# Kernel tuning notes

Hardware: AMD Instinct MI355X
Metric: run time of the kernel (lower is better)

Reference implementation:

```python
import jax, jax.numpy as jnp
import numpy as np
from jax import lax

# Dimensions (must match input_specs)
B, T, C = 2, 2048, 1024
H = 4 * C          # FFN hidden
E_RWKV, E_TRANS = 6, 2
E = E_RWKV + E_TRANS
LN_EPS = 1e-5


def layernorm(x, g, b):
    m = x.mean(-1, keepdims=True)
    v = ((x - m) ** 2).mean(-1, keepdims=True)
    return (x - m) * lax.rsqrt(v + LN_EPS) * g + b


def setup_inputs() -> dict:
    key = jax.random.key(0)
    ks = jax.random.split(key, 24)
    s = 0.02
    inp = {
        "x": jax.random.normal(ks[0], (B, T, C), jnp.float32),
        "v_first": jax.random.normal(ks[1], (B, T, C), jnp.float32),
        "winners": jax.random.randint(ks[2], (B, T, 2), 0, E),
        "capital_shares": jax.random.uniform(ks[3], (E,), jnp.float32),
        # LayerNorms
        "ln1_g": jnp.ones((C,), jnp.float32), "ln1_b": jnp.zeros((C,), jnp.float32),
        "ln2_g": jnp.ones((C,), jnp.float32), "ln2_b": jnp.zeros((C,), jnp.float32),
        # RWKV-style time-mix (simplified RWKV7_TimeMix)
        "Wr": s * jax.random.normal(ks[4], (C, C), jnp.float32),
        "Wk": s * jax.random.normal(ks[5], (C, C), jnp.float32),
        "Wv": s * jax.random.normal(ks[6], (C, C), jnp.float32),
        "Wo": s * jax.random.normal(ks[7], (C, C), jnp.float32),
        "w_decay": jax.random.normal(ks[8], (C,), jnp.float32),
        "g_v": jax.random.normal(ks[9], (C,), jnp.float32),
        # bridge: linear on concat(h, rwkv_state)
        "Wb": s * jax.random.normal(ks[10], (2 * C, C), jnp.float32),
        "bb": jnp.zeros((C,), jnp.float32),
        # 6 stacked SparseRWKVFFN experts: sigmoid(x Wr_r) * (relu(x Wk_r)^2 Wv_r)
        "Wk_r": s * jax.random.normal(ks[11], (E_RWKV, C, H), jnp.float32),
        "Wv_r": s * jax.random.normal(ks[12], (E_RWKV, H, C), jnp.float32),
        "Wr_r": s * jax.random.normal(ks[13], (E_RWKV, C, C), jnp.float32),
        # 2 stacked LinearTransformerExpert: gelu((h+prefix) W1) W2
        "W1_t": s * jax.random.normal(ks[14], (E_TRANS, C, H), jnp.float32),
        "W2_t": s * jax.random.normal(ks[15], (E_TRANS, H, C), jnp.float32),
    }
    return inp


def reference(x, v_first, winners, capital_shares,
              ln1_g, ln1_b, ln2_g, ln2_b,
              Wr, Wk, Wv, Wo, w_decay, g_v,
              Wb, bb, Wk_r, Wv_r, Wr_r, W1_t, W2_t):
    # ---- attention (simplified RWKV time-mix), returns per-token state ----
    h1 = layernorm(x, ln1_g, ln1_b)
    r = jax.nn.sigmoid(h1 @ Wr)                      # [B,T,C]
    k = h1 @ Wk
    v = h1 @ Wv
    v = v + (v_first - v) * jax.nn.sigmoid(g_v)      # value-residual mix
    w = jax.nn.sigmoid(w_decay)                      # per-channel decay [C]

    def step(s, kv):
        k_t, v_t = kv                                # [B,C] each
        s = w * s + k_t * v_t
        return s, s

    s0 = jnp.zeros((B, C), x.dtype)
    _, states = lax.scan(step, s0, (jnp.swapaxes(k, 0, 1), jnp.swapaxes(v, 0, 1)))
    states = jnp.swapaxes(states, 0, 1)              # rwkv_state [B,T,C]

    att_out = (r * states) @ Wo
    x = x + att_out
    h = layernorm(x, ln2_g, ln2_b)

    # ---- bridge prefix (flat over tokens, vectorized) ----
    bridge_prefix = jnp.concatenate([h, states], axis=-1) @ Wb + bb  # [B,T,C]

    # ---- experts computed densely, combined by top-2 gates ----
    # RWKV FFN experts
    a = jnp.square(jax.nn.relu(jnp.einsum('btc,ech->ebth', h, Wk_r)))     # [Er,B,T,H]
    rec = jax.nn.sigmoid(jnp.einsum('btc,ecd->ebtd', h, Wr_r))            # [Er,B,T,C]
    out_r = rec * jnp.einsum('ebth,ehc->ebtc', a, Wv_r)                   # [Er,B,T,C]
    # Linear-transformer experts consume the bridge prefix
    ht = h + bridge_prefix
    out_t = jnp.einsum('ebth,ehc->ebtc',
                       jax.nn.gelu(jnp.einsum('btc,ech->ebth', ht, W1_t)),
                       W2_t)                                              # [Et,B,T,C]
    all_out = jnp.concatenate([out_r, out_t], axis=0)                     # [E,B,T,C]

    # top-2 combine, each rank weighted 0.5 (use_market=False branch)
    gate = 0.5 * (jax.nn.one_hot(winners[..., 0], E, dtype=x.dtype)
                  + jax.nn.one_hot(winners[..., 1], E, dtype=x.dtype))    # [B,T,E]
    final_out = jnp.einsum('ebtc,bte->btc', all_out, gate)

    return x + final_out
```

## Files before the change

kernel.cpp:

```cpp
#include <hip/hip_runtime.h>

typedef unsigned short u16;
typedef __bf16 bf16x8 __attribute__((ext_vector_type(8)));
typedef float f32x4 __attribute__((ext_vector_type(4)));

__device__ __forceinline__ float bf2f(u16 u){ union{unsigned i;float f;}x; x.i=((unsigned)u)<<16; return x.f; }
__device__ __forceinline__ u16 f2bf(float f){ union{float f;unsigned i;}x; x.f=f; unsigned r = x.i + 0x7FFFu + ((x.i>>16)&1u); return (u16)(r>>16); }
__device__ __forceinline__ float sigm(float x){ return 1.f/(1.f+expf(-x)); }

struct __align__(8) U16x4 { u16 v[4]; };

__global__ void conv_t(const float* __restrict__ src, u16* __restrict__ dst, int K, int N){
  __shared__ u16 tile[64][72];
  const size_t mo = (size_t)blockIdx.z * (size_t)K * (size_t)N;
  src += mo; dst += mo;
  int k0 = blockIdx.x*64, n0 = blockIdx.y*64;
  int tid = threadIdx.x;
  #pragma unroll
  for (int it=0; it<4; ++it){
    int e = it*1024 + tid*4;
    int r = e>>6, c = e&63;
    float4 v = *(const float4*)(src + (size_t)(k0+r)*N + n0 + c);
    tile[r][c+0]=f2bf(v.x); tile[r][c+1]=f2bf(v.y); tile[r][c+2]=f2bf(v.z); tile[r][c+3]=f2bf(v.w);
  }
  __syncthreads();
  #pragma unroll
  for (int it=0; it<4; ++it){
    int e = it*1024 + tid*4;
    int n = e>>6, k = e&63;
    U16x4 o;
    #pragma unroll
    for (int j=0;j<4;++j) o.v[j] = tile[k+j][n];
    *(U16x4*)(dst + (size_t)(n0+n)*K + k0 + k) = o;
  }
}

__global__ void ln_k(const float* __restrict__ x, const float* __restrict__ g, const float* __restrict__ b,
                     u16* __restrict__ out, int ostride){
  int row = blockIdx.x, tid = threadIdx.x;
  float4 v = *(const float4*)(x + (size_t)row*1024 + tid*4);
  float s = v.x+v.y+v.z+v.w;
  float ss = v.x*v.x+v.y*v.y+v.z*v.z+v.w*v.w;
  #pragma unroll
  for (int o=32;o;o>>=1){ s += __shfl_down(s,o); ss += __shfl_down(ss,o); }
  __shared__ float sm[8];
  int lane = tid&63, wv = tid>>6;
  if (!lane){ sm[wv]=s; sm[4+wv]=ss; }
  __syncthreads();
  s = sm[0]+sm[1]+sm[2]+sm[3]; ss = sm[4]+sm[5]+sm[6]+sm[7];
  float mean = s*(1.f/1024.f);
  float var = ss*(1.f/1024.f) - mean*mean;
  float inv = rsqrtf(var + 1e-5f);
  U16x4 o;
  const float* vp = &v.x;
  #pragma unroll
  for (int j=0;j<4;++j){
    int c = tid*4+j;
    o.v[j] = f2bf((vp[j]-mean)*inv*g[c] + b[c]);
  }
  *(U16x4*)(out + (size_t)row*ostride + tid*4) = o;
}

__global__ void scan_p1(const u16* __restrict__ kbuf, const u16* __restrict__ vbuf,
                        const float* __restrict__ w_decay, float* __restrict__ carry){
  int c = blockIdx.x*256 + threadIdx.x;
  int chunk = blockIdx.y, b = blockIdx.z;
  float w = sigm(w_decay[c]);
  float s = 0.f;
  size_t idx = ((size_t)(b*2048 + chunk*64))*1024 + c;
  #pragma unroll 4
  for (int i=0;i<64;++i){ s = w*s + bf2f(kbuf[idx])*bf2f(vbuf[idx]); idx += 1024; }
  carry[((size_t)(b*32+chunk))*1024 + c] = s;
}
__global__ void scan_p2(const float* __restrict__ w_decay, const float* __restrict__ carry,
                        float* __restrict__ startv){
  int c = blockIdx.x*256 + threadIdx.x;
  int b = blockIdx.y;
  float w = sigm(w_decay[c]);
  float wL = w;
  #pragma unroll
  for (int i=0;i<6;++i) wL *= wL;
  float p = 0.f;
  for (int j=0;j<32;++j){
    size_t id = ((size_t)(b*32+j))*1024 + c;
    startv[id] = p;
    p = wL*p + carry[id];
  }
}
__global__ void scan_p3(const u16* __restrict__ kbuf, const u16* __restrict__ vbuf, const u16* __restrict__ rbuf,
                        const float* __restrict__ w_decay, const float* __restrict__ startv,
                        u16* __restrict__ rs, u16* __restrict__ hcat){
  int c = blockIdx.x*256 + threadIdx.x;
  int chunk = blockIdx.y, b = blockIdx.z;
  float w = sigm(w_decay[c]);
  float s = startv[((size_t)(b*32+chunk))*1024 + c];
  size_t t0 = (size_t)b*2048 + chunk*64;
  size_t idx = t0*1024 + c;
  size_t idx2 = t0*2048 + 1024 + c;
  for (int i=0;i<64;++i){
    s = w*s + bf2f(kbuf[idx])*bf2f(vbuf[idx]);
    rs[idx] = f2bf(bf2f(rbuf[idx]) * s);
    hcat[idx2] = f2bf(s);
    idx += 1024; idx2 += 2048;
  }
}

__global__ void route_count(const int* __restrict__ winners, int* __restrict__ offs, int* __restrict__ cursor){
  __shared__ int cnt[8];
  if (threadIdx.x < 8) cnt[threadIdx.x] = 0;
  __syncthreads();
  for (int p = threadIdx.x; p < 8192; p += 256) atomicAdd(&cnt[winners[p]&7], 1);
  __syncthreads();
  if (threadIdx.x == 0){
    int s = 0;
    #pragma unroll
    for (int e=0;e<8;++e){ offs[e]=s; s+=cnt[e]; }
    offs[8]=s;
  }
  if (threadIdx.x < 8) cursor[threadIdx.x] = 0;
}
__global__ void route_scatter(const int* __restrict__ winners, const int* __restrict__ offs,
                              int* __restrict__ cursor, int* __restrict__ idx_all){
  int p = blockIdx.x*256 + threadIdx.x;
  if (p < 8192){
    int e = winners[p]&7;
    int pos = offs[e] + atomicAdd(&cursor[e], 1);
    idx_all[pos] = p>>1;
  }
}

struct GArgs {
  const u16* A; const u16* B;
  long long lda, bstride;
  int K, N, Mdense, eBase;
  const int* offs; const int* idx_all;
  const float* x; const float* v_first; const float* g_v;
  u16* rbuf; u16* kbuf; u16* vbuf;
  float* out;
  const u16* hcat; const float* bb; u16* ht;
  u16* act; u16* rec;
};

#define GLL(gp, lp) __builtin_amdgcn_global_load_lds((const __attribute__((address_space(1))) void*)(gp), \
                                                     (__attribute__((address_space(3))) void*)(lp), 16, 0, 0)

template<int EPI, int GATHER>
__global__ __launch_bounds__(256,2) void gemm_k(GArgs g){
  int e = g.eBase + blockIdx.z;
  int rbase = 0, m = g.Mdense;
  if (g.offs){ rbase = g.offs[e]; m = g.offs[e+1] - rbase; }
  if ((int)blockIdx.y * 128 >= m) return;
  __shared__ char smem[65536];
  const int tid = threadIdx.x, lane = tid&63, wave = tid>>6;
  const int wr = wave>>1, wc = wave&1;

  int srow[4], scol[4];
  #pragma unroll
  for (int i=0;i<4;++i){
    srow[i] = i*32 + (tid>>3);
    scol[i] = ((((tid&7)*16) ^ ((srow[i]&7)<<4)) >> 1);
  }
  const u16* bBase[4];
  #pragma unroll
  for (int i=0;i<4;++i)
    bBase[i] = g.B + (long long)blockIdx.z*g.bstride
             + ((long long)blockIdx.x*128 + srow[i])*(long long)g.K + scol[i];

  int aOff[4][2], bOff[4][2];
  #pragma unroll
  for (int mm=0;mm<4;++mm){
    int rm = wr*64 + mm*16 + (lane&15);
    int rn = wc*64 + mm*16 + (lane&15);
    #pragma unroll
    for (int kk=0;kk<2;++kk){
      int X = kk*64 + (lane>>4)*16;
      aOff[mm][kk] = rm*128 + (X ^ ((rm&7)<<4));
      bOff[mm][kk] = 16384 + rn*128 + (X ^ ((rn&7)<<4));
    }
  }
  char* ldsA = smem + wave*1024;
  char* ldsB = smem + 16384 + wave*1024;
  const int nk = g.K >> 6;

  for (int mt = blockIdx.y; mt*128 < m; mt += gridDim.y){
    const u16* aSrc[4]; const u16* bSrc[4];
    #pragma unroll
    for (int i=0;i<4;++i){
      int grow = mt*128 + srow[i];
      int lr = grow < m ? grow : m-1;
      long long arow;
      if (GATHER) arow = g.idx_all[rbase + lr];
      else if (g.offs) arow = rbase + lr;
      else arow = grow;
      aSrc[i] = g.A + arow*g.lda + scol[i];
      bSrc[i] = bBase[i];
    }
    f32x4 acc[4][4];
    #pragma unroll
    for (int mm=0;mm<4;++mm)
      #pragma unroll
      for (int nn=0;nn<4;++nn)
        acc[mm][nn] = f32x4{0.f,0.f,0.f,0.f};

    #pragma unroll
    for (int i=0;i<4;++i){
      GLL(aSrc[i], ldsA + i*4096);
      GLL(bSrc[i], ldsB + i*4096);
      aSrc[i] += 64; bSrc[i] += 64;
    }
    int cur = 0;
    for (int ks=0; ks<nk; ++ks){
      if (ks+1 < nk){
        int nb = (cur^1)*32768;
        #pragma unroll
        for (int i=0;i<4;++i){
          GLL(aSrc[i], ldsA + nb + i*4096);
          GLL(bSrc[i], ldsB + nb + i*4096);
          aSrc[i] += 64; bSrc[i] += 64;
        }
        asm volatile("s_waitcnt vmcnt(8)" ::: "memory");
      } else {
        asm volatile("s_waitcnt vmcnt(0)" ::: "memory");
      }
      asm volatile("s_barrier" ::: "memory");
      const char* base = smem + cur*32768;
      #pragma unroll
      for (int kk=0;kk<2;++kk){
        bf16x8 af[4], bfv[4];
        #pragma unroll
        for (int q=0;q<4;++q) af[q] = *(const bf16x8*)(base + aOff[q][kk]);
        #pragma unroll
        for (int q=0;q<4;++q) bfv[q] = *(const bf16x8*)(base + bOff[q][kk]);
        #pragma unroll
        for (int mm=0;mm<4;++mm)
          #pragma unroll
          for (int nn=0;nn<4;++nn)
            acc[mm][nn] = __builtin_amdgcn_mfma_f32_16x16x32_bf16(af[mm], bfv[nn], acc[mm][nn], 0,0,0);
      }
      asm volatile("s_waitcnt lgkmcnt(0)" ::: "memory");
      asm volatile("s_barrier" ::: "memory");
      cur ^= 1;
    }

    int colBase = blockIdx.x*128 + wc*64 + (lane&15);
    #pragma unroll
    for (int mm=0;mm<4;++mm){
      #pragma unroll
      for (int j=0;j<4;++j){
        int grow = mt*128 + wr*64 + mm*16 + (lane>>4)*4 + j;
        if (grow >= m) continue;
        size_t t = (size_t)grow;
        int gr = rbase + grow;
        #pragma unroll
        for (int nn=0;nn<4;++nn){
          int col = colBase + nn*16;
          float val = acc[mm][nn][j];
          if (EPI==0){
            if (col < 1024) g.rbuf[t*1024+col] = f2bf(sigm(val));
            else if (col < 2048) g.kbuf[t*1024+col-1024] = f2bf(val);
            else {
              int c2 = col-2048;
              float sg = sigm(g.g_v[c2]);
              float vf = g.v_first[t*1024+c2];
              g.vbuf[t*1024+c2] = f2bf(val + (vf-val)*sg);
            }
          } else if (EPI==1){
            g.out[t*1024+col] = g.x[t*1024+col] + val;
          } else if (EPI==2){
            g.ht[t*1024+col] = f2bf(bf2f(g.hcat[t*2048+col]) + val + g.bb[col]);
          } else if (EPI==3){
            float r_ = fmaxf(val, 0.f);
            g.act[(size_t)gr*4096+col] = f2bf(r_*r_);
          } else if (EPI==4){
            g.rec[(size_t)gr*1024+col] = f2bf(sigm(val));
          } else if (EPI==5){
            int tok = g.idx_all[gr];
            float rc = bf2f(g.rec[(size_t)gr*1024+col]);
            atomicAdd(&g.out[(size_t)tok*1024+col], 0.5f*val*rc);
          } else if (EPI==6){
            float t3 = val*val*val;
            float th = tanhf(0.79788456080286535588f*(val + 0.044715f*t3));
            g.act[(size_t)gr*4096+col] = f2bf(0.5f*val*(1.f+th));
          } else if (EPI==7){
            int tok = g.idx_all[gr];
            atomicAdd(&g.out[(size_t)tok*1024+col], 0.5f*val);
          }
        }
      }
    }
  }
}

extern "C" void kernel_launch(void* const* d_in, const int* in_sizes, int n_in,
                              void* d_out, int out_size, void* d_ws, size_t ws_size,
                              hipStream_t stream) {
  const float* x       = (const float*)d_in[0];
  const float* v_first = (const float*)d_in[1];
  const int*   winners = (const int*)d_in[2];
  const float* ln1_g   = (const float*)d_in[4];
  const float* ln1_b   = (const float*)d_in[5];
  const float* ln2_g   = (const float*)d_in[6];
  const float* ln2_b   = (const float*)d_in[7];
  const float* Wr      = (const float*)d_in[8];
  const float* Wk      = (const float*)d_in[9];
  const float* Wv      = (const float*)d_in[10];
  const float* Wo      = (const float*)d_in[11];
  const float* w_decay = (const float*)d_in[12];
  const float* g_v     = (const float*)d_in[13];
  const float* Wb      = (const float*)d_in[14];
  const float* bb      = (const float*)d_in[15];
  const float* Wk_r    = (const float*)d_in[16];
  const float* Wv_r    = (const float*)d_in[17];
  const float* Wr_r    = (const float*)d_in[18];
  const float* W1_t    = (const float*)d_in[19];
  const float* W2_t    = (const float*)d_in[20];
  float* out = (float*)d_out;

  char* p = (char*)d_ws;
  auto alloc = [&](size_t bytes)->char*{ char* r=p; p += (bytes+255)&~(size_t)255; return r; };
  u16* wTrkv = (u16*)alloc(3072ull*1024*2);
  u16* wTo   = (u16*)alloc(1024ull*1024*2);
  u16* wTb   = (u16*)alloc(1024ull*2048*2);
  u16* wTkr  = (u16*)alloc(6ull*4096*1024*2);
  u16* wTvr  = (u16*)alloc(6ull*1024*4096*2);
  u16* wTrr  = (u16*)alloc(6ull*1024*1024*2);
  u16* wT1   = (u16*)alloc(2ull*4096*1024*2);
  u16* wT2   = (u16*)alloc(2ull*1024*4096*2);
  u16* h1    = (u16*)alloc(4096ull*1024*2);
  u16* rbuf  = (u16*)alloc(4096ull*1024*2);
  u16* kbuf  = (u16*)alloc(4096ull*1024*2);
  u16* vbuf  = (u16*)alloc(4096ull*1024*2);
  u16* rsb   = (u16*)alloc(4096ull*1024*2);
  u16* hcat  = (u16*)alloc(4096ull*2048*2);
  u16* htb   = (u16*)alloc(4096ull*1024*2);
  u16* act   = (u16*)alloc(8192ull*4096*2);
  u16* rec   = (u16*)alloc(8192ull*1024*2);
  float* carry  = (float*)alloc(2ull*32*1024*4);
  float* startv = (float*)alloc(2ull*32*1024*4);
  int* offs   = (int*)alloc(16*4);
  int* cursor = (int*)alloc(8*4);
  int* idx_all= (int*)alloc(8192*4);

  dim3 B256(256);

  conv_t<<<dim3(16,16,1),B256,0,stream>>>(Wr,   wTrkv,            1024,1024);
  conv_t<<<dim3(16,16,1),B256,0,stream>>>(Wk,   wTrkv+1024*1024,  1024,1024);
  conv_t<<<dim3(16,16,1),B256,0,stream>>>(Wv,   wTrkv+2048*1024,  1024,1024);
  conv_t<<<dim3(16,16,1),B256,0,stream>>>(Wo,   wTo,              1024,1024);
  conv_t<<<dim3(32,16,1),B256,0,stream>>>(Wb,   wTb,              2048,1024);
  conv_t<<<dim3(16,64,6),B256,0,stream>>>(Wk_r, wTkr,             1024,4096);
  conv_t<<<dim3(64,16,6),B256,0,stream>>>(Wv_r, wTvr,             4096,1024);
  conv_t<<<dim3(16,16,6),B256,0,stream>>>(Wr_r, wTrr,             1024,1024);
  conv_t<<<dim3(16,64,2),B256,0,stream>>>(W1_t, wT1,              1024,4096);
  conv_t<<<dim3(64,16,2),B256,0,stream>>>(W2_t, wT2,              4096,1024);

  route_count<<<1,B256,0,stream>>>(winners, offs, cursor);
  route_scatter<<<32,B256,0,stream>>>(winners, offs, cursor, idx_all);

  ln_k<<<4096,B256,0,stream>>>(x, ln1_g, ln1_b, h1, 1024);

  {
    GArgs ga{}; ga.A=h1; ga.B=wTrkv; ga.lda=1024; ga.bstride=0; ga.K=1024; ga.N=3072; ga.Mdense=4096;
    ga.v_first=v_first; ga.g_v=g_v; ga.rbuf=rbuf; ga.kbuf=kbuf; ga.vbuf=vbuf;
    gemm_k<0,0><<<dim3(24,32,1),B256,0,stream>>>(ga);
  }

  scan_p1<<<dim3(4,32,2),B256,0,stream>>>(kbuf, vbuf, w_decay, carry);
  scan_p2<<<dim3(4,2,1), B256,0,stream>>>(w_decay, carry, startv);
  scan_p3<<<dim3(4,32,2),B256,0,stream>>>(kbuf, vbuf, rbuf, w_decay, startv, rsb, hcat);

  {
    GArgs ga{}; ga.A=rsb; ga.B=wTo; ga.lda=1024; ga.K=1024; ga.N=1024; ga.Mdense=4096;
    ga.x=x; ga.out=out;
    gemm_k<1,0><<<dim3(8,32,1),B256,0,stream>>>(ga);
  }

  ln_k<<<4096,B256,0,stream>>>(out, ln2_g, ln2_b, hcat, 2048);

  {
    GArgs ga{}; ga.A=hcat; ga.B=wTb; ga.lda=2048; ga.K=2048; ga.N=1024; ga.Mdense=4096;
    ga.hcat=hcat; ga.bb=bb; ga.ht=htb;
    gemm_k<2,0><<<dim3(8,32,1),B256,0,stream>>>(ga);
  }

  {
    GArgs ga{}; ga.A=hcat; ga.B=wTkr; ga.lda=2048; ga.bstride=4096ll*1024; ga.K=1024; ga.N=4096;
    ga.offs=offs; ga.eBase=0; ga.idx_all=idx_all; ga.act=act;
    gemm_k<3,1><<<dim3(32,12,6),B256,0,stream>>>(ga);
  }
  {
    GArgs ga{}; ga.A=hcat; ga.B=wTrr; ga.lda=2048; ga.bstride=1024ll*1024; ga.K=1024; ga.N=1024;
    ga.offs=offs; ga.eBase=0; ga.idx_all=idx_all; ga.rec=rec;
    gemm_k<4,1><<<dim3(8,12,6),B256,0,stream>>>(ga);
  }
  {
    GArgs ga{}; ga.A=act; ga.B=wTvr; ga.lda=4096; ga.bstride=1024ll*4096; ga.K=4096; ga.N=1024;
    ga.offs=offs; ga.eBase=0; ga.idx_all=idx_all; ga.rec=rec; ga.out=out;
    gemm_k<5,0><<<dim3(8,12,6),B256,0,stream>>>(ga);
  }
  {
    GArgs ga{}; ga.A=htb; ga.B=wT1; ga.lda=1024; ga.bstride=4096ll*1024; ga.K=1024; ga.N=4096;
    ga.offs=offs; ga.eBase=6; ga.idx_all=idx_all; ga.act=act;
    gemm_k<6,1><<<dim3(32,12,2),B256,0,stream>>>(ga);
  }
  {
    GArgs ga{}; ga.A=act; ga.B=wT2; ga.lda=4096; ga.bstride=1024ll*4096; ga.K=4096; ga.N=1024;
    ga.offs=offs; ga.eBase=6; ga.idx_all=idx_all; ga.out=out;
    gemm_k<7,0><<<dim3(8,12,2),B256,0,stream>>>(ga);
  }

  (void)in_sizes; (void)n_in; (void)out_size; (void)ws_size;
}
```

Baseline: 753.7 us.

## Add split-K with bf16 partials, 3-stage K32 pipeline, and fused weight conversion

Measured after the change: 736.8 us. -2.2%, faster.

```diff
diff --git a/kernel.cpp b/kernel.cpp
--- a/kernel.cpp
+++ b/kernel.cpp
@@ -10,11 +10,23 @@
 
 struct __align__(8) U16x4 { u16 v[4]; };
 
-__global__ void conv_t(const float* __restrict__ src, u16* __restrict__ dst, int K, int N){
+#define PSTRIDE 8388608ull
+
+struct CJob { const float* src; u16* dst; int K, N, base; };
+struct CJobs { CJob j[27]; };
+
+__global__ void conv_all(CJobs cj){
   __shared__ u16 tile[64][72];
-  const size_t mo = (size_t)blockIdx.z * (size_t)K * (size_t)N;
-  src += mo; dst += mo;
-  int k0 = blockIdx.x*64, n0 = blockIdx.y*64;
+  int id = blockIdx.x;
+  int sel = 0;
+  #pragma unroll
+  for (int i=1;i<27;++i) if (cj.j[i].base <= id) sel = i;
+  const float* __restrict__ src = cj.j[sel].src;
+  u16* __restrict__ dst = cj.j[sel].dst;
+  int K = cj.j[sel].K, N = cj.j[sel].N;
+  int lt = id - cj.j[sel].base;
+  int tn = N >> 6;
+  int k0 = (lt / tn) * 64, n0 = (lt % tn) * 64;
   int tid = threadIdx.x;
   #pragma unroll
   for (int it=0; it<4; ++it){
@@ -132,69 +144,59 @@
 struct GArgs {
   const u16* A; const u16* B;
   long long lda, bstride;
-  int K, N, Mdense, eBase;
+  int K, Mdense, eBase, nxt, kdiv;
   const int* offs; const int* idx_all;
-  const float* x; const float* v_first; const float* g_v;
+  const float* v_first; const float* g_v;
   u16* rbuf; u16* kbuf; u16* vbuf;
-  float* out;
-  const u16* hcat; const float* bb; u16* ht;
-  u16* act; u16* rec;
+  u16* act; u16* part;
 };
 
 #define GLL(gp, lp) __builtin_amdgcn_global_load_lds((const __attribute__((address_space(1))) void*)(gp), \
                                                      (__attribute__((address_space(3))) void*)(lp), 16, 0, 0)
 
 template<int EPI, int GATHER>
-__global__ __launch_bounds__(256,2) void gemm_k(GArgs g){
+__global__ __launch_bounds__(256,3) void gemm_k(GArgs g){
   int e = g.eBase + blockIdx.z;
   int rbase = 0, m = g.Mdense;
   if (g.offs){ rbase = g.offs[e]; m = g.offs[e+1] - rbase; }
   if ((int)blockIdx.y * 128 >= m) return;
-  __shared__ char smem[65536];
+  const int xt = (int)blockIdx.x % g.nxt;
+  const int ksplit = (int)blockIdx.x / g.nxt;
+  const long long kOff = (long long)ksplit * g.kdiv;
+  __shared__ char smem[49152];
   const int tid = threadIdx.x, lane = tid&63, wave = tid>>6;
   const int wr = wave>>1, wc = wave&1;
-
-  int srow[4], scol[4];
-  #pragma unroll
-  for (int i=0;i<4;++i){
-    srow[i] = i*32 + (tid>>3);
-    scol[i] = ((((tid&7)*16) ^ ((srow[i]&7)<<4)) >> 1);
-  }
-  const u16* bBase[4];
-  #pragma unroll
-  for (int i=0;i<4;++i)
-    bBase[i] = g.B + (long long)blockIdx.z*g.bstride
-             + ((long long)blockIdx.x*128 + srow[i])*(long long)g.K + scol[i];
-
-  int aOff[4][2], bOff[4][2];
-  #pragma unroll
-  for (int mm=0;mm<4;++mm){
-    int rm = wr*64 + mm*16 + (lane&15);
-    int rn = wc*64 + mm*16 + (lane&15);
-    #pragma unroll
-    for (int kk=0;kk<2;++kk){
-      int X = kk*64 + (lane>>4)*16;
-      aOff[mm][kk] = rm*128 + (X ^ ((rm&7)<<4));
-      bOff[mm][kk] = 16384 + rn*128 + (X ^ ((rn&7)<<4));
+  const int nk = g.kdiv >> 5;
+
+  const int srowi = tid>>2;
+  const long long scol = (long long)((tid&3)*8);
+
+  const u16* bBase0 = g.B + (long long)blockIdx.z*g.bstride
+                    + ((long long)(xt*128) + srowi)*(long long)g.K + kOff + scol;
+  const u16* bBase1 = bBase0 + 64ll*(long long)g.K;
+
+  int aRd[4], bRd[4];
+  #pragma unroll
+  for (int q=0;q<4;++q){
+    aRd[q] = (wr*64 + q*16 + (lane&15))*64 + (lane>>4)*16;
+    bRd[q] = 8192 + (wc*64 + q*16 + (lane&15))*64 + (lane>>4)*16;
+  }
+
+  for (int mt = blockIdx.y; mt*128 < m; mt += gridDim.y){
+    const u16 *aP0, *aP1;
+    {
+      int g0 = mt*128 + srowi;       g0 = g0 < m ? g0 : m-1;
+      int g1 = mt*128 + 64 + srowi;  g1 = g1 < m ? g1 : m-1;
+      long long r0, r1;
+      if (GATHER){ r0 = g.idx_all[rbase+g0]; r1 = g.idx_all[rbase+g1]; }
+      else if (g.offs){ r0 = rbase+g0; r1 = rbase+g1; }
+      else { r0 = g0; r1 = g1; }
+      aP0 = g.A + r0*g.lda + kOff + scol;
+      aP1 = g.A + r1*g.lda + kOff + scol;
     }
-  }
-  char* ldsA = smem + wave*1024;
-  char* ldsB = smem + 16384 + wave*1024;
-  const int nk = g.K >> 6;
-
-  for (int mt = blockIdx.y; mt*128 < m; mt += gridDim.y){
-    const u16* aSrc[4]; const u16* bSrc[4];
-    #pragma unroll
-    for (int i=0;i<4;++i){
-      int grow = mt*128 + srow[i];
-      int lr = grow < m ? grow : m-1;
-      long long arow;
-      if (GATHER) arow = g.idx_all[rbase + lr];
-      else if (g.offs) arow = rbase + lr;
-      else arow = grow;
-      aSrc[i] = g.A + arow*g.lda + scol[i];
-      bSrc[i] = bBase[i];
-    }
+    const u16* bP0 = bBase0;
+    const u16* bP1 = bBase1;
+
     f32x4 acc[4][4];
     #pragma unroll
     for (int mm=0;mm<4;++mm)
@@ -202,92 +204,129 @@
       for (int nn=0;nn<4;++nn)
         acc[mm][nn] = f32x4{0.f,0.f,0.f,0.f};
 
-    #pragma unroll
-    for (int i=0;i<4;++i){
-      GLL(aSrc[i], ldsA + i*4096);
-      GLL(bSrc[i], ldsB + i*4096);
-      aSrc[i] += 64; bSrc[i] += 64;
-    }
-    int cur = 0;
+    #define STAGE(BUF) do{ \
+      char* db = smem + (BUF)*16384 + wave*1024; \
+      GLL(aP0, db); GLL(aP1, db+4096); GLL(bP0, db+8192); GLL(bP1, db+12288); \
+      aP0+=32; aP1+=32; bP0+=32; bP1+=32; }while(0)
+
+    STAGE(0); STAGE(1);
+    int bufC = 0, bufS = 2;
     for (int ks=0; ks<nk; ++ks){
-      if (ks+1 < nk){
-        int nb = (cur^1)*32768;
-        #pragma unroll
-        for (int i=0;i<4;++i){
-          GLL(aSrc[i], ldsA + nb + i*4096);
-          GLL(bSrc[i], ldsB + nb + i*4096);
-          aSrc[i] += 64; bSrc[i] += 64;
-        }
+      if (ks+2 < nk){
+        STAGE(bufS); bufS = bufS==2 ? 0 : bufS+1;
         asm volatile("s_waitcnt vmcnt(8)" ::: "memory");
+      } else if (ks+1 < nk){
+        asm volatile("s_waitcnt vmcnt(4)" ::: "memory");
       } else {
         asm volatile("s_waitcnt vmcnt(0)" ::: "memory");
       }
       asm volatile("s_barrier" ::: "memory");
-      const char* base = smem + cur*32768;
+      const char* base = smem + bufC*16384;
+      bf16x8 af[4], bfv[4];
       #pragma unroll
-      for (int kk=0;kk<2;++kk){
-        bf16x8 af[4], bfv[4];
+      for (int q=0;q<4;++q) af[q] = *(const bf16x8*)(base + aRd[q]);
+      #pragma unroll
+      for (int q=0;q<4;++q) bfv[q] = *(const bf16x8*)(base + bRd[q]);
+      #pragma unroll
+      for (int mm=0;mm<4;++mm)
         #pragma unroll
-        for (int q=0;q<4;++q) af[q] = *(const bf16x8*)(base + aOff[q][kk]);
-        #pragma unroll
-        for (int q=0;q<4;++q) bfv[q] = *(const bf16x8*)(base + bOff[q][kk]);
-        #pragma unroll
-        for (int mm=0;mm<4;++mm)
-          #pragma unroll
-          for (int nn=0;nn<4;++nn)
-            acc[mm][nn] = __builtin_amdgcn_mfma_f32_16x16x32_bf16(af[mm], bfv[nn], acc[mm][nn], 0,0,0);
-      }
+        for (int nn=0;nn<4;++nn)
+          acc[mm][nn] = __builtin_amdgcn_mfma_f32_16x16x32_bf16(af[mm], bfv[nn], acc[mm][nn], 0,0,0);
       asm volatile("s_waitcnt lgkmcnt(0)" ::: "memory");
       asm volatile("s_barrier" ::: "memory");
-      cur ^= 1;
+      bufC = bufC==2 ? 0 : bufC+1;
     }
-
-    int colBase = blockIdx.x*128 + wc*64 + (lane&15);
+    #undef STAGE
+
+    int colB = xt*128 + wc*64 + (lane&15);
     #pragma unroll
     for (int mm=0;mm<4;++mm){
       #pragma unroll
       for (int j=0;j<4;++j){
         int grow = mt*128 + wr*64 + mm*16 + (lane>>4)*4 + j;
         if (grow >= m) continue;
-        size_t t = (size_t)grow;
-        int gr = rbase + grow;
+        size_t gr = (size_t)(rbase + grow);
         #pragma unroll
         for (int nn=0;nn<4;++nn){
-          int col = colBase + nn*16;
+          int col = colB + nn*16;
           float val = acc[mm][nn][j];
           if (EPI==0){
-            if (col < 1024) g.rbuf[t*1024+col] = f2bf(sigm(val));
-            else if (col < 2048) g.kbuf[t*1024+col-1024] = f2bf(val);
+            if (col < 1024) g.rbuf[gr*1024+col] = f2bf(sigm(val));
+            else if (col < 2048) g.kbuf[gr*1024+col-1024] = f2bf(val);
             else {
               int c2 = col-2048;
               float sg = sigm(g.g_v[c2]);
-              float vf = g.v_first[t*1024+c2];
-              g.vbuf[t*1024+c2] = f2bf(val + (vf-val)*sg);
+              float vf = g.v_first[gr*1024+c2];
+              g.vbuf[gr*1024+c2] = f2bf(val + (vf-val)*sg);
             }
-          } else if (EPI==1){
-            g.out[t*1024+col] = g.x[t*1024+col] + val;
-          } else if (EPI==2){
-            g.ht[t*1024+col] = f2bf(bf2f(g.hcat[t*2048+col]) + val + g.bb[col]);
           } else if (EPI==3){
             float r_ = fmaxf(val, 0.f);
-            g.act[(size_t)gr*4096+col] = f2bf(r_*r_);
-          } else if (EPI==4){
-            g.rec[(size_t)gr*1024+col] = f2bf(sigm(val));
-          } else if (EPI==5){
-            int tok = g.idx_all[gr];
-            float rc = bf2f(g.rec[(size_t)gr*1024+col]);
-            atomicAdd(&g.out[(size_t)tok*1024+col], 0.5f*val*rc);
+            g.act[gr*4096+col] = f2bf(r_*r_);
           } else if (EPI==6){
             float t3 = val*val*val;
             float th = tanhf(0.79788456080286535588f*(val + 0.044715f*t3));
-            g.act[(size_t)gr*4096+col] = f2bf(0.5f*val*(1.f+th));
-          } else if (EPI==7){
-            int tok = g.idx_all[gr];
-            atomicAdd(&g.out[(size_t)tok*1024+col], 0.5f*val);
+            g.act[gr*4096+col] = f2bf(0.5f*val*(1.f+th));
+          } else {
+            g.part[(size_t)ksplit*PSTRIDE + gr*1024 + col] = f2bf(val);
           }
         }
       }
     }
+  }
+}
+
+__global__ void red_add_x(const float* __restrict__ x, const u16* __restrict__ part, float* __restrict__ out){
+  size_t i = (size_t)blockIdx.x*1024 + threadIdx.x*4;
+  U16x4 p0 = *(const U16x4*)(part + i);
+  U16x4 p1 = *(const U16x4*)(part + PSTRIDE + i);
+  float4 xv = *(const float4*)(x + i);
+  float4 o;
+  o.x = xv.x + bf2f(p0.v[0]) + bf2f(p1.v[0]);
+  o.y = xv.y + bf2f(p0.v[1]) + bf2f(p1.v[1]);
+  o.z = xv.z + bf2f(p0.v[2]) + bf2f(p1.v[2]);
+  o.w = xv.w + bf2f(p0.v[3]) + bf2f(p1.v[3]);
+  *(float4*)(out + i) = o;
+}
+__global__ void red_ht(const u16* __restrict__ hcat, const u16* __restrict__ part,
+                       const float* __restrict__ bb, u16* __restrict__ ht){
+  int c = threadIdx.x*4;
+  size_t i = (size_t)blockIdx.x*1024 + c;
+  U16x4 p0 = *(const U16x4*)(part + i);
+  U16x4 p1 = *(const U16x4*)(part + PSTRIDE + i);
+  U16x4 hv = *(const U16x4*)(hcat + (size_t)blockIdx.x*2048 + c);
+  U16x4 o;
+  #pragma unroll
+  for (int j=0;j<4;++j) o.v[j] = f2bf(bf2f(hv.v[j]) + bf2f(p0.v[j]) + bf2f(p1.v[j]) + bb[c+j]);
+  *(U16x4*)(ht + i) = o;
+}
+__global__ void red_rec(const int* __restrict__ offs, const u16* __restrict__ part, u16* __restrict__ rec){
+  int r = blockIdx.x;
+  if (r >= offs[6]) return;
+  size_t i = (size_t)r*1024 + threadIdx.x*4;
+  U16x4 p0 = *(const U16x4*)(part + i);
+  U16x4 p1 = *(const U16x4*)(part + PSTRIDE + i);
+  U16x4 o;
+  #pragma unroll
+  for (int j=0;j<4;++j) o.v[j] = f2bf(sigm(bf2f(p0.v[j]) + bf2f(p1.v[j])));
+  *(U16x4*)(rec + i) = o;
+}
+__global__ void red_moe(const int* __restrict__ offs, const int* __restrict__ idx_all,
+                        const u16* __restrict__ part, const u16* __restrict__ rec, float* __restrict__ out){
+  int gr = blockIdx.x;
+  if (gr >= offs[8]) return;
+  int tok = idx_all[gr];
+  bool isr = gr < offs[6];
+  int c = threadIdx.x*4;
+  size_t i = (size_t)gr*1024 + c;
+  U16x4 p0 = *(const U16x4*)(part + i);
+  U16x4 p1 = *(const U16x4*)(part + PSTRIDE + i);
+  U16x4 rv;
+  if (isr) rv = *(const U16x4*)(rec + i);
+  #pragma unroll
+  for (int j=0;j<4;++j){
+    float s = bf2f(p0.v[j]) + bf2f(p1.v[j]);
+    float v = isr ? 0.5f*s*bf2f(rv.v[j]) : 0.5f*s;
+    atomicAdd(&out[(size_t)tok*1024 + c + j], v);
   }
 }
 
@@ -335,6 +374,7 @@
   u16* htb   = (u16*)alloc(4096ull*1024*2);
   u16* act   = (u16*)alloc(8192ull*4096*2);
   u16* rec   = (u16*)alloc(8192ull*1024*2);
+  u16* partial = (u16*)alloc(2ull*8192*1024*2);
   float* carry  = (float*)alloc(2ull*32*1024*4);
   float* startv = (float*)alloc(2ull*32*1024*4);
   int* offs   = (int*)alloc(16*4);
@@ -343,16 +383,21 @@
 
   dim3 B256(256);
 
-  conv_t<<<dim3(16,16,1),B256,0,stream>>>(Wr,   wTrkv,            1024,1024);
-  conv_t<<<dim3(16,16,1),B256,0,stream>>>(Wk,   wTrkv+1024*1024,  1024,1024);
-  conv_t<<<dim3(16,16,1),B256,0,stream>>>(Wv,   wTrkv+2048*1024,  1024,1024);
-  conv_t<<<dim3(16,16,1),B256,0,stream>>>(Wo,   wTo,              1024,1024);
-  conv_t<<<dim3(32,16,1),B256,0,stream>>>(Wb,   wTb,              2048,1024);
-  conv_t<<<dim3(16,64,6),B256,0,stream>>>(Wk_r, wTkr,             1024,4096);
-  conv_t<<<dim3(64,16,6),B256,0,stream>>>(Wv_r, wTvr,             4096,1024);
-  conv_t<<<dim3(16,16,6),B256,0,stream>>>(Wr_r, wTrr,             1024,1024);
-  conv_t<<<dim3(16,64,2),B256,0,stream>>>(W1_t, wT1,              1024,4096);
-  conv_t<<<dim3(64,16,2),B256,0,stream>>>(W2_t, wT2,              4096,1024);
+  {
+    CJobs cj; int base = 0, ji = 0;
+    auto add = [&](const float* s, u16* d, int K, int N){
+      cj.j[ji++] = CJob{s, d, K, N, base}; base += (K>>6)*(N>>6);
+    };
+    add(Wr, wTrkv, 1024,1024); add(Wk, wTrkv+1024*1024, 1024,1024);
+    add(Wv, wTrkv+2048*1024, 1024,1024); add(Wo, wTo, 1024,1024);
+    add(Wb, wTb, 2048,1024);
+    for (int e2=0;e2<6;++e2) add(Wk_r + (size_t)e2*1024*4096, wTkr + (size_t)e2*4096*1024, 1024,4096);
+    for (int e2=0;e2<6;++e2) add(Wv_r + (size_t)e2*4096*1024, wTvr + (size_t)e2*1024*4096, 4096,1024);
+    for (int e2=0;e2<6;++e2) add(Wr_r + (size_t)e2*1024*1024, wTrr + (size_t)e2*1024*1024, 1024,1024);
+    for (int e2=0;e2<2;++e2) add(W1_t + (size_t)e2*1024*4096, wT1 + (size_t)e2*4096*1024, 1024,4096);
+    for (int e2=0;e2<2;++e2) add(W2_t + (size_t)e2*4096*1024, wT2 + (size_t)e2*1024*4096, 4096,1024);
+    conv_all<<<dim3(base,1,1),B256,0,stream>>>(cj);
+  }
 
   route_count<<<1,B256,0,stream>>>(winners, offs, cursor);
   route_scatter<<<32,B256,0,stream>>>(winners, offs, cursor, idx_all);
@@ -360,7 +405,7 @@
   ln_k<<<4096,B256,0,stream>>>(x, ln1_g, ln1_b, h1, 1024);
 
   {
-    GArgs ga{}; ga.A=h1; ga.B=wTrkv; ga.lda=1024; ga.bstride=0; ga.K=1024; ga.N=3072; ga.Mdense=4096;
+    GArgs ga{}; ga.A=h1; ga.B=wTrkv; ga.lda=1024; ga.K=1024; ga.Mdense=4096; ga.nxt=24; ga.kdiv=1024;
     ga.v_first=v_first; ga.g_v=g_v; ga.rbuf=rbuf; ga.kbuf=kbuf; ga.vbuf=vbuf;
     gemm_k<0,0><<<dim3(24,32,1),B256,0,stream>>>(ga);
   }
@@ -370,44 +415,49 @@
   scan_p3<<<dim3(4,32,2),B256,0,stream>>>(kbuf, vbuf, rbuf, w_decay, startv, rsb, hcat);
 
   {
-    GArgs ga{}; ga.A=rsb; ga.B=wTo; ga.lda=1024; ga.K=1024; ga.N=1024; ga.Mdense=4096;
-    ga.x=x; ga.out=out;
-    gemm_k<1,0><<<dim3(8,32,1),B256,0,stream>>>(ga);
-  }
+    GArgs ga{}; ga.A=rsb; ga.B=wTo; ga.lda=1024; ga.K=1024; ga.Mdense=4096; ga.nxt=8; ga.kdiv=512;
+    ga.part=partial;
+    gemm_k<1,0><<<dim3(16,32,1),B256,0,stream>>>(ga);
+  }
+  red_add_x<<<4096,B256,0,stream>>>(x, partial, out);
 
   ln_k<<<4096,B256,0,stream>>>(out, ln2_g, ln2_b, hcat, 2048);
 
   {
-    GArgs ga{}; ga.A=hcat; ga.B=wTb; ga.lda=2048; ga.K=2048; ga.N=1024; ga.Mdense=4096;
-    ga.hcat=hcat; ga.bb=bb; ga.ht=htb;
-    gemm_k<2,0><<<dim3(8,32,1),B256,0,stream>>>(ga);
-  }
-
-  {
-    GArgs ga{}; ga.A=hcat; ga.B=wTkr; ga.lda=2048; ga.bstride=4096ll*1024; ga.K=1024; ga.N=4096;
+    GArgs ga{}; ga.A=hcat; ga.B=wTb; ga.lda=2048; ga.K=2048; ga.Mdense=4096; ga.nxt=8; ga.kdiv=1024;
+    ga.part=partial;
+    gemm_k<2,0><<<dim3(16,32,1),B256,0,stream>>>(ga);
+  }
+  red_ht<<<4096,B256,0,stream>>>(hcat, partial, bb, htb);
+
+  {
+    GArgs ga{}; ga.A=hcat; ga.B=wTkr; ga.lda=2048; ga.bstride=4096ll*1024; ga.K=1024; ga.nxt=32; ga.kdiv=1024;
     ga.offs=offs; ga.eBase=0; ga.idx_all=idx_all; ga.act=act;
     gemm_k<3,1><<<dim3(32,12,6),B256,0,stream>>>(ga);
   }
   {
-    GArgs ga{}; ga.A=hcat; ga.B=wTrr; ga.lda=2048; ga.bstride=1024ll*1024; ga.K=1024; ga.N=1024;
-    ga.offs=offs; ga.eBase=0; ga.idx_all=idx_all; ga.rec=rec;
-    gemm_k<4,1><<<dim3(8,12,6),B256,0,stream>>>(ga);
-  }
-  {
-    GArgs ga{}; ga.A=act; ga.B=wTvr; ga.lda=4096; ga.bstride=1024ll*4096; ga.K=4096; ga.N=1024;
-    ga.offs=offs; ga.eBase=0; ga.idx_all=idx_all; ga.rec=rec; ga.out=out;
-    gemm_k<5,0><<<dim3(8,12,6),B256,0,stream>>>(ga);
-  }
-  {
-    GArgs ga{}; ga.A=htb; ga.B=wT1; ga.lda=1024; ga.bstride=4096ll*1024; ga.K=1024; ga.N=4096;
+    GArgs ga{}; ga.A=hcat; ga.B=wTrr; ga.lda=2048; ga.bstride=1024ll*1024; ga.K=1024; ga.nxt=8; ga.kdiv=512;
+    ga.offs=offs; ga.eBase=0; ga.idx_all=idx_all; ga.part=partial;
+    gemm_k<4,1><<<dim3(16,12,6),B256,0,stream>>>(ga);
+  }
+  red_rec<<<8192,B256,0,stream>>>(offs, partial, rec);
+
+  {
+    GArgs ga{}; ga.A=act; ga.B=wTvr; ga.lda=4096; ga.bstride=1024ll*4096; ga.K=4096; ga.nxt=8; ga.kdiv=2048;
+    ga.offs=offs; ga.eBase=0; ga.part=partial;
+    gemm_k<5,0><<<dim3(16,12,6),B256,0,stream>>>(ga);
+  }
+  {
+    GArgs ga{}; ga.A=htb; ga.B=wT1; ga.lda=1024; ga.bstride=4096ll*1024; ga.K=1024; ga.nxt=32; ga.kdiv=1024;
     ga.offs=offs; ga.eBase=6; ga.idx_all=idx_all; ga.act=act;
-    gemm_k<6,1><<<dim3(32,12,2),B256,0,stream>>>(ga);
-  }
-  {
-    GArgs ga{}; ga.A=act; ga.B=wT2; ga.lda=4096; ga.bstride=1024ll*4096; ga.K=4096; ga.N=1024;
-    ga.offs=offs; ga.eBase=6; ga.idx_all=idx_all; ga.out=out;
-    gemm_k<7,0><<<dim3(8,12,2),B256,0,stream>>>(ga);
-  }
+    gemm_k<6,1><<<dim3(32,16,2),B256,0,stream>>>(ga);
+  }
+  {
+    GArgs ga{}; ga.A=act; ga.B=wT2; ga.lda=4096; ga.bstride=1024ll*4096; ga.K=4096; ga.nxt=8; ga.kdiv=2048;
+    ga.offs=offs; ga.eBase=6; ga.part=partial;
+    gemm_k<7,0><<<dim3(16,16,2),B256,0,stream>>>(ga);
+  }
+  red_moe<<<8192,B256,0,stream>>>(offs, idx_all, partial, rec, out);
 
   (void)in_sizes; (void)n_in; (void)out_size; (void)ws_size;
 }
```
